# Performance work log

Measured on AMD Instinct MI355X. Metric: run time of the kernel, lower is better.

Reference implementation:

```python
import jax, jax.numpy as jnp
import numpy as np

TAU = 2.0      # LIF membrane time constant
VTH = 1.0      # spike threshold
ALPHA = 2.0    # surrogate-gradient sharpness (atan surrogate)
EPS = 1e-5     # BatchNorm eps

@jax.custom_vjp
def spike(u):
    return (u > 0.0).astype(u.dtype)

def _spike_fwd(u):
    return spike(u), u

def _spike_bwd(u, g):
    sg = ALPHA / (2.0 * (1.0 + (jnp.pi / 2.0 * ALPHA * u) ** 2))
    return (g * sg,)

spike.defvjp(_spike_fwd, _spike_bwd)

def lif_time(x):
    # x: [B,T,C,H,W] -> spikes [B,T,C,H,W]; hard-reset LIF, v0 = 0
    xT = jnp.moveaxis(x, 1, 0)  # [T,B,C,H,W]
    def step(v, xt):
        v = v + (xt - v) / TAU
        s = spike(v - VTH)
        return v * (1.0 - s), s
    _, sT = jax.lax.scan(step, jnp.zeros_like(xT[0]), xT)
    return jnp.moveaxis(sT, 0, 1)

def conv2d(x, w, stride, pad):
    return jax.lax.conv_general_dilated(
        x, w, (stride, stride), [(pad, pad), (pad, pad)],
        dimension_numbers=('NCHW', 'OIHW', 'NCHW'))

def bn(x, gamma, beta, mean, var):
    # inference-style BatchNorm2d with running stats; x: [N,C,H,W]
    inv = gamma * jax.lax.rsqrt(var + EPS)
    return x * inv[None, :, None, None] + (beta - mean * inv)[None, :, None, None]

def setup_inputs() -> dict:
    key = jax.random.key(0)
    ks = jax.random.split(key, 16)
    B, T, Cin, Cout, H, W = 16, 8, 128, 256, 56, 56
    d = {}
    d['x_spike'] = (jax.random.uniform(ks[0], (B, T, Cin, H, W)) < 0.2).astype(jnp.float32)
    d['conv1_w'] = jax.random.normal(ks[1], (Cout, Cin, 3, 3), dtype=jnp.float32) * 0.05
    d['conv2_w'] = jax.random.normal(ks[2], (Cout, Cout, 3, 3), dtype=jnp.float32) * 0.05
    d['ds_w'] = jax.random.normal(ks[3], (Cout, Cin, 1, 1), dtype=jnp.float32) * 0.05
    for i, p in enumerate(['n1', 'n2', 'nd']):
        d[p + '_gamma'] = 1.0 + 0.1 * jax.random.normal(ks[4 + i], (Cout,), dtype=jnp.float32)
        d[p + '_beta'] = 0.1 * jax.random.normal(ks[7 + i], (Cout,), dtype=jnp.float32)
        d[p + '_mean'] = 0.01 * jax.random.normal(ks[10 + i], (Cout,), dtype=jnp.float32)
        d[p + '_var'] = jax.random.uniform(ks[13 + i], (Cout,), minval=0.5, maxval=1.5)
    return d

def reference(x_spike, conv1_w, conv2_w, ds_w,
              n1_gamma, n1_beta, n1_mean, n1_var,
              n2_gamma, n2_beta, n2_mean, n2_var,
              nd_gamma, nd_beta, nd_mean, nd_var):
    B, T, Cin, H, W = x_spike.shape
    x_flat = x_spike.reshape(B * T, Cin, H, W)
    # downsample shortcut (1x1 conv stride 2 + BN)
    identity = bn(conv2d(x_flat, ds_w, 2, 0), nd_gamma, nd_beta, nd_mean, nd_var)
    # NOTE: original module runs lif_shortcut on identity but DISCARDS the result
    # (pure state side-effect); it does not affect the output, so it is omitted.
    out = bn(conv2d(x_flat, conv1_w, 2, 1), n1_gamma, n1_beta, n1_mean, n1_var)
    Cout, Ho, Wo = out.shape[1], out.shape[2], out.shape[3]
    out = lif_time(out.reshape(B, T, Cout, Ho, Wo))
    out = bn(conv2d(out.reshape(B * T, Cout, Ho, Wo), conv2_w, 1, 1),
             n2_gamma, n2_beta, n2_mean, n2_var) + identity
    return lif_time(out.reshape(B, T, Cout, Ho, Wo))
```

## Files before the change

### kernel.cpp

```cpp
#include <hip/hip_runtime.h>
#include <hip/hip_bf16.h>

#define CIN  128
#define CO   256
#define HIN  56
#define WIN  56
#define OH   28
#define OWW  28
#define P    784
#define HWIN 3136
#define PERT 200704

typedef __attribute__((ext_vector_type(8))) short bf16x8v;
typedef __attribute__((ext_vector_type(4))) float f32x4;

__device__ __forceinline__ f32x4 mfma16(bf16x8v a, bf16x8v b, f32x4 c) {
    return __builtin_amdgcn_mfma_f32_16x16x32_bf16(a, b, c, 0, 0, 0);
}

__device__ __forceinline__ void gld_lds16(const void* g, void* l) {
    __builtin_amdgcn_global_load_lds(
        (const __attribute__((address_space(1))) void*)g,
        (__attribute__((address_space(3))) void*)l, 16, 0, 0);
}

__global__ __launch_bounds__(256) void k_prep_bias(
    const float* __restrict__ g1, const float* __restrict__ b1,
    const float* __restrict__ m1, const float* __restrict__ v1,
    const float* __restrict__ g2, const float* __restrict__ b2,
    const float* __restrict__ m2, const float* __restrict__ v2,
    const float* __restrict__ gd, const float* __restrict__ bd,
    const float* __restrict__ md, const float* __restrict__ vd,
    float* __restrict__ inv1o, float* __restrict__ bias1o,
    float* __restrict__ inv2o, float* __restrict__ invdo,
    float* __restrict__ bias2o)
{
    int co = threadIdx.x;
    float inv1 = g1[co] / sqrtf(v1[co] + 1e-5f);
    float inv2 = g2[co] / sqrtf(v2[co] + 1e-5f);
    float invd = gd[co] / sqrtf(vd[co] + 1e-5f);
    inv1o[co]  = inv1;
    bias1o[co] = fmaf(-m1[co], inv1, b1[co]);
    inv2o[co]  = inv2;
    invdo[co]  = invd;
    bias2o[co] = fmaf(-m2[co], inv2, b2[co]) + fmaf(-md[co], invd, bd[co]);
}

__global__ __launch_bounds__(256) void k_prep_w2p(
    const float* __restrict__ w2, const float* __restrict__ inv2,
    unsigned short* __restrict__ hi, unsigned short* __restrict__ lo)
{
    int i = blockIdx.x * 256 + threadIdx.x;
    if (i >= 73728) return;
    int tap = i >> 13;
    int r   = i & 8191;
    int ch  = r >> 10;
    int r2  = r & 1023;
    int cf  = r2 >> 6;
    int lane = r2 & 63;
    int co  = cf * 16 + (lane & 15);
    int cib = ch * 32 + (lane >> 4) * 8;
#pragma unroll
    for (int j = 0; j < 8; j++) {
        float w = w2[((size_t)co * CO + cib + j) * 9 + tap] * inv2[co];
        __hip_bfloat16 h = __float2bfloat16(w);
        __hip_bfloat16 l = __float2bfloat16(w - __bfloat162float(h));
        hi[(size_t)i * 8 + j] = *(unsigned short*)&h;
        lo[(size_t)i * 8 + j] = *(unsigned short*)&l;
    }
}

__global__ __launch_bounds__(256) void k_prep_w1p(
    const float* __restrict__ w1, const float* __restrict__ inv1,
    unsigned short* __restrict__ hi, unsigned short* __restrict__ mid,
    unsigned short* __restrict__ lo)
{
    int i = blockIdx.x * 256 + threadIdx.x;
    if (i >= 36864) return;
    int tap = i >> 12;
    int r   = i & 4095;
    int ch  = r >> 10;
    int r2  = r & 1023;
    int cf  = r2 >> 6;
    int lane = r2 & 63;
    int co  = cf * 16 + (lane & 15);
    int cib = ch * 32 + (lane >> 4) * 8;
#pragma unroll
    for (int j = 0; j < 8; j++) {
        float w = w1[((size_t)co * CIN + cib + j) * 9 + tap] * inv1[co];
        __hip_bfloat16 h = __float2bfloat16(w);
        float r1 = w - __bfloat162float(h);
        __hip_bfloat16 m = __float2bfloat16(r1);
        float r2f = r1 - __bfloat162float(m);
        __hip_bfloat16 l = __float2bfloat16(r2f);
        hi[(size_t)i * 8 + j]  = *(unsigned short*)&h;
        mid[(size_t)i * 8 + j] = *(unsigned short*)&m;
        lo[(size_t)i * 8 + j]  = *(unsigned short*)&l;
    }
}

__global__ __launch_bounds__(256) void k_prep_wdp(
    const float* __restrict__ wd, const float* __restrict__ invd,
    unsigned short* __restrict__ hi, unsigned short* __restrict__ lo)
{
    int i = blockIdx.x * 256 + threadIdx.x;
    if (i >= 4096) return;
    int ch  = i >> 10;
    int r2  = i & 1023;
    int cf  = r2 >> 6;
    int lane = r2 & 63;
    int co  = cf * 16 + (lane & 15);
    int cib = ch * 32 + (lane >> 4) * 8;
#pragma unroll
    for (int j = 0; j < 8; j++) {
        float w = wd[(size_t)co * CIN + cib + j] * invd[co];
        __hip_bfloat16 h = __float2bfloat16(w);
        __hip_bfloat16 l = __float2bfloat16(w - __bfloat162float(h));
        hi[(size_t)i * 8 + j] = *(unsigned short*)&h;
        lo[(size_t)i * 8 + j] = *(unsigned short*)&l;
    }
}

__global__ __launch_bounds__(256) void k_pack1(
    const float* __restrict__ x, unsigned int* __restrict__ xt_p)
{
    int i = blockIdx.x * 256 + threadIdx.x;
    int pos = i % HWIN;
    int nw  = i / HWIN;
    int w   = nw & 3;
    int n   = nw >> 2;
    const float* xp = x + ((size_t)n * CIN + w * 32) * HWIN + pos;
    unsigned int word = 0;
#pragma unroll
    for (int ci = 0; ci < 32; ci++)
        if (xp[(size_t)ci * HWIN] != 0.f) word |= (1u << ci);
    xt_p[((size_t)n * HWIN + pos) * 4 + w] = word;
}

__global__ __launch_bounds__(256) void k_conv1_mfma(
    const unsigned int* __restrict__ xt_p,
    const unsigned short* __restrict__ w1hip,
    const unsigned short* __restrict__ w1midp,
    const unsigned short* __restrict__ w1lop,
    const float* __restrict__ bias1,
    float* __restrict__ out)
{
    __shared__ unsigned int XW[4 * 522];

    const int n    = blockIdx.x / 7;
    const int rt   = blockIdx.x - n * 7;
    const int r0   = rt * 4;
    const int tid  = threadIdx.x;
    const int wave = tid >> 6;
    const int lane = tid & 63;
    const int l15  = lane & 15;
    const int quad = lane >> 4;
    const int cf0  = blockIdx.y * 8 + wave * 2;

    const unsigned int* xp_n = xt_p + (size_t)n * HWIN * 4;
    for (int i = tid; i < 513; i += 256) {
        int row = i / 57, c = i - row * 57;
        int irow = 2 * r0 - 1 + row;
        int iw   = c - 1;
        uint4 val = {0u, 0u, 0u, 0u};
        if (irow >= 0 && iw >= 0)
            val = *(const uint4*)(xp_n + (size_t)(irow * WIN + iw) * 4);
        int base = row * 58 + c;
        XW[0 * 522 + base] = val.x;
        XW[1 * 522 + base] = val.y;
        XW[2 * 522 + base] = val.z;
        XW[3 * 522 + base] = val.w;
    }
    __syncthreads();

    int rr[7], cc[7];
#pragma unroll
    for (int f = 0; f < 7; f++) {
        int pos = f * 16 + l15;
        rr[f] = pos / 28;
        cc[f] = pos - rr[f] * 28;
    }

    f32x4 acc[2][7];
#pragma unroll
    for (int g = 0; g < 2; g++)
#pragma unroll
        for (int f = 0; f < 7; f++) acc[g][f] = (f32x4){0.f, 0.f, 0.f, 0.f};

    bf16x8v ch0, cm0, cl0, ch1, cm1, cl1;
    bf16x8v nh0, nm0, nl0, nh1, nm1, nl1;
    {
        size_t b0 = ((size_t)0 * 16 + cf0) * 512 + lane * 8;
        ch0 = *(const bf16x8v*)(w1hip + b0);  cm0 = *(const bf16x8v*)(w1midp + b0);
        cl0 = *(const bf16x8v*)(w1lop + b0);
        ch1 = *(const bf16x8v*)(w1hip + b0 + 512); cm1 = *(const bf16x8v*)(w1midp + b0 + 512);
        cl1 = *(const bf16x8v*)(w1lop + b0 + 512);
        nh0 = ch0; nm0 = cm0; nl0 = cl0; nh1 = ch1; nm1 = cm1; nl1 = cl1;
    }

    for (int c = 0; c < 4; c++) {
        for (int tap = 0; tap < 9; tap++) {
            int rd = c * 9 + tap;
            if (rd < 35) {
                int rn = rd + 1, cn = rn / 9, tn = rn - cn * 9;
                size_t b0 = ((size_t)(tn * 4 + cn) * 16 + cf0) * 512 + lane * 8;
                nh0 = *(const bf16x8v*)(w1hip + b0);  nm0 = *(const bf16x8v*)(w1midp + b0);
                nl0 = *(const bf16x8v*)(w1lop + b0);
                nh1 = *(const bf16x8v*)(w1hip + b0 + 512); nm1 = *(const bf16x8v*)(w1midp + b0 + 512);
                nl1 = *(const bf16x8v*)(w1lop + b0 + 512);
            }
            const int kh = tap / 3, kw = tap - kh * 3;
#pragma unroll
            for (int f = 0; f < 7; f++) {
                unsigned int word = XW[c * 522 + (2 * rr[f] + kh) * 58 + 2 * cc[f] + kw];
                unsigned int byt  = (word >> (quad * 8)) & 0xffu;
                uint4 u;
                u.x = ((byt & 1u)   ? 0x3F80u : 0u) | ((byt & 2u)   ? 0x3F800000u : 0u);
                u.y = ((byt & 4u)   ? 0x3F80u : 0u) | ((byt & 8u)   ? 0x3F800000u : 0u);
                u.z = ((byt & 16u)  ? 0x3F80u : 0u) | ((byt & 32u)  ? 0x3F800000u : 0u);
                u.w = ((byt & 64u)  ? 0x3F80u : 0u) | ((byt & 128u) ? 0x3F800000u : 0u);
                union { uint4 q; bf16x8v v; } cv;
                cv.q = u;
                acc[0][f] = mfma16(ch0, cv.v, acc[0][f]);
                acc[0][f] = mfma16(cm0, cv.v, acc[0][f]);
                acc[0][f] = mfma16(cl0, cv.v, acc[0][f]);
                acc[1][f] = mfma16(ch1, cv.v, acc[1][f]);
                acc[1][f] = mfma16(cm1, cv.v, acc[1][f]);
                acc[1][f] = mfma16(cl1, cv.v, acc[1][f]);
            }
            ch0 = nh0; cm0 = nm0; cl0 = nl0; ch1 = nh1; cm1 = nm1; cl1 = nl1;
        }
    }

#pragma unroll
    for (int g = 0; g < 2; g++)
#pragma unroll
        for (int f = 0; f < 7; f++) {
            int pg = rt * 112 + f * 16 + l15;
#pragma unroll
            for (int reg = 0; reg < 4; reg++) {
                int co = cf0 * 16 + g * 16 + quad * 4 + reg;
                out[((size_t)n * CO + co) * P + pg] = acc[g][f][reg] + bias1[co];
            }
        }
}

__global__ __launch_bounds__(256) void k_lif1t(
    const float* __restrict__ pre, unsigned short* __restrict__ st)
{
    __shared__ unsigned short T[16 * 68];
    const int b   = blockIdx.x;
    const int co0 = blockIdx.y * 64;
    const int p0  = blockIdx.z * 16;
    const int tid  = threadIdx.x;
    const int pcol = tid & 15;
    const int g    = tid >> 4;
    const int pos = p0 + g;
    const int oh  = pos / 28, ow = pos - oh * 28;
    const int f8  = ((((oh + 1) * 30 + ow + 1) >> 1) & 3);
    const int o      = (pcol & 7) >> 1;
    const int no     = o ^ f8;
    const int within = (pcol & 1) * 4;
    const int chp    = (co0 >> 5) + (pcol >> 3);
    float v[4] = {0.f, 0.f, 0.f, 0.f};
    for (int t = 0; t < 8; t++) {
        const float* src = pre + (((size_t)(b * 8 + t)) * CO + co0) * P + p0;
        unsigned short s[4];
#pragma unroll
        for (int j = 0; j < 4; j++) {
            int co = g + 16 * j;
            float xv = src[(size_t)co * P + pcol];
            v[j] = v[j] + (xv - v[j]) * 0.5f;
            bool sp = v[j] > 1.0f;
            s[j] = sp ? 0x3F80 : 0;
            if (sp) v[j] = 0.f;
        }
        __syncthreads();
#pragma unroll
        for (int j = 0; j < 4; j++) T[pcol * 68 + g + 16 * j] = s[j];
        __syncthreads();
        unsigned short* dst = st + (((size_t)(b * 8 + t) * 8 + chp) * P + pos) * 32
                               + no * 8 + within;
        ushort4 ov;
        ov.x = T[g * 68 + pcol * 4 + 0];
        ov.y = T[g * 68 + pcol * 4 + 1];
        ov.z = T[g * 68 + pcol * 4 + 2];
        ov.w = T[g * 68 + pcol * 4 + 3];
        *(ushort4*)dst = ov;
    }
}

__global__ __launch_bounds__(256) void k_conv2_mfma(
    const unsigned short* __restrict__ spike_t,
    const unsigned int* __restrict__ xt_p,
    const unsigned short* __restrict__ w2hip,
    const unsigned short* __restrict__ w2lop,
    const unsigned short* __restrict__ wdhip,
    const unsigned short* __restrict__ wdlop,
    const float* __restrict__ bias2,
    float* __restrict__ out)
{
    __shared__ unsigned short SB[2 * 5760];
    __shared__ unsigned int   XW2[4 * 112];

    const int n    = blockIdx.x / 7;
    const int rt   = blockIdx.x - n * 7;
    const int r0   = rt * 4;
    const int tid  = threadIdx.x;
    const int wave = tid >> 6;
    const int lane = tid & 63;
    const int l15  = lane & 15;
    const int quad = lane >> 4;
    const int cf0  = blockIdx.y * 8 + wave * 2;

    {
        uint4 z = {0u, 0u, 0u, 0u};
        for (int i = tid; i < 1440; i += 256) ((uint4*)SB)[i] = z;
    }
    for (int i = tid; i < 112; i += 256) {
        int r = i / 28, c = i - r * 28;
        uint4 w4 = *(const uint4*)(xt_p + ((size_t)n * HWIN
                    + (2 * (r0 + r)) * WIN + 2 * c) * 4);
        XW2[0 * 112 + i] = w4.x;
        XW2[1 * 112 + i] = w4.y;
        XW2[2 * 112 + i] = w4.z;
        XW2[3 * 112 + i] = w4.w;
    }
    __syncthreads();

    int  g_irow[3], g_lds[3];
    bool g_ok[3];
    int  g_half[3];
#pragma unroll
    for (int k = 0; k < 3; k++) {
        int idx  = wave * 3 + k;
        int row  = idx >> 1, half = idx & 1;
        int irow = r0 - 1 + row;
        g_irow[k] = irow;
        g_half[k] = half;
        g_ok[k]   = ((unsigned)irow < 28u) && (half == 0 || lane < 48);
        g_lds[k]  = row * 1920 + 64 + half * 1024;
    }
    const char* sp_n = (const char*)spike_t + (size_t)n * 8 * P * 64;

#pragma unroll
    for (int k = 0; k < 3; k++)
        if (g_ok[k])
            gld_lds16(sp_n + (size_t)g_irow[k] * 1792 + g_half[k] * 1024 + lane * 16,
                      (char*)SB + g_lds[k]);

    int rr[7], cc[7];
#pragma unroll
    for (int f = 0; f < 7; f++) {
        int pos = f * 16 + l15;
        rr[f] = pos / 28;
        cc[f] = pos - rr[f] * 28;
    }

    f32x4 acc[2][7];
#pragma unroll
    for (int g = 0; g < 2; g++)
#pragma unroll
        for (int f = 0; f < 7; f++) acc[g][f] = (f32x4){0.f, 0.f, 0.f, 0.f};

    for (int c = 0; c < 4; c++) {
        size_t b0 = ((size_t)c * 16 + cf0) * 512 + lane * 8;
        bf16x8v a0h = *(const bf16x8v*)(wdhip + b0);
        bf16x8v a0l = *(const bf16x8v*)(wdlop + b0);
        bf16x8v a1h = *(const bf16x8v*)(wdhip + b0 + 512);
        bf16x8v a1l = *(const bf16x8v*)(wdlop + b0 + 512);
#pragma unroll
        for (int f = 0; f < 7; f++) {
            unsigned int word = XW2[c * 112 + rr[f] * 28 + cc[f]];
            unsigned int byt  = (word >> (quad * 8)) & 0xffu;
            uint4 u;
            u.x = ((byt & 1u)   ? 0x3F80u : 0u) | ((byt & 2u)   ? 0x3F800000u : 0u);
            u.y = ((byt & 4u)   ? 0x3F80u : 0u) | ((byt & 8u)   ? 0x3F800000u : 0u);
            u.z = ((byt & 16u)  ? 0x3F80u : 0u) | ((byt & 32u)  ? 0x3F800000u : 0u);
            u.w = ((byt & 64u)  ? 0x3F80u : 0u) | ((byt & 128u) ? 0x3F800000u : 0u);
            union { uint4 q; bf16x8v v; } cv;
            cv.q = u;
            acc[0][f] = mfma16(a0h, cv.v, acc[0][f]);
            acc[0][f] = mfma16(a0l, cv.v, acc[0][f]);
            acc[1][f] = mfma16(a1h, cv.v, acc[1][f]);
            acc[1][f] = mfma16(a1l, cv.v, acc[1][f]);
        }
    }
    __syncthreads();

    bf16x8v ch0, cl0, ch1, cl1, nh0, nl0, nh1, nl1;
    {
        size_t b0 = ((size_t)0 * 16 + cf0) * 512 + lane * 8;
        ch0 = *(const bf16x8v*)(w2hip + b0);
        cl0 = *(const bf16x8v*)(w2lop + b0);
        ch1 = *(const bf16x8v*)(w2hip + b0 + 512);
        cl1 = *(const bf16x8v*)(w2lop + b0 + 512);
        nh0 = ch0; nl0 = cl0; nh1 = ch1; nl1 = cl1;
    }

    for (int c = 0; c < 8; c++) {
        if (c < 7) {
            const char* base = sp_n + (size_t)(c + 1) * 50176;
            char* dstb = (char*)SB + ((c + 1) & 1) * 11520;
#pragma unroll
            for (int k = 0; k < 3; k++)
                if (g_ok[k])
                    gld_lds16(base + (size_t)g_irow[k] * 1792 + g_half[k] * 1024 + lane * 16,
                              dstb + g_lds[k]);
        }
        const int bufsh = (c & 1) * 5760;
        for (int tap = 0; tap < 9; tap++) {
            int rd = c * 9 + tap;
            if (rd < 71) {
                int rn = rd + 1, cn = rn / 9, tn = rn - cn * 9;
                size_t b0 = ((size_t)(tn * 8 + cn) * 16 + cf0) * 512 + lane * 8;
                nh0 = *(const bf16x8v*)(w2hip + b0);
                nl0 = *(const bf16x8v*)(w2lop + b0);
                nh1 = *(const bf16x8v*)(w2hip + b0 + 512);
                nl1 = *(const bf16x8v*)(w2lop + b0 + 512);
            }
            const int kh = tap / 3, kw = tap - kh * 3;
#pragma unroll
            for (int f = 0; f < 7; f++) {
                int slot = (rr[f] + kh) * 30 + cc[f] + kw;
                int sw   = (slot >> 1) & 3;
                bf16x8v bfr = *(const bf16x8v*)(
                    &SB[bufsh + slot * 32 + ((quad ^ sw) * 8)]);
                acc[0][f] = mfma16(ch0, bfr, acc[0][f]);
                acc[0][f] = mfma16(cl0, bfr, acc[0][f]);
                acc[1][f] = mfma16(ch1, bfr, acc[1][f]);
                acc[1][f] = mfma16(cl1, bfr, acc[1][f]);
            }
            ch0 = nh0; cl0 = nl0; ch1 = nh1; cl1 = nl1;
        }
        __syncthreads();
    }

#pragma unroll
    for (int g = 0; g < 2; g++)
#pragma unroll
        for (int f = 0; f < 7; f++) {
            int pg = rt * 112 + f * 16 + l15;
#pragma unroll
            for (int reg = 0; reg < 4; reg++) {
                int co = cf0 * 16 + g * 16 + quad * 4 + reg;
                out[((size_t)n * CO + co) * P + pg] = acc[g][f][reg] + bias2[co];
            }
        }
}

__global__ __launch_bounds__(256) void k_lif4(const float4* __restrict__ in,
                                              float4* __restrict__ out)
{
    const int q = PERT / 4;
    const int i = blockIdx.x * 256 + threadIdx.x;
    const int b = i / q;
    const int r = i - b * q;
    const float4* pi = in  + (size_t)(b * 8) * q + r;
    float4*       po = out + (size_t)(b * 8) * q + r;
    float v0 = 0.f, v1 = 0.f, v2 = 0.f, v3 = 0.f;
#pragma unroll
    for (int t = 0; t < 8; t++) {
        float4 xt = pi[(size_t)t * q];
        float4 s;
        v0 = v0 + (xt.x - v0) * 0.5f; s.x = (v0 > 1.0f) ? 1.f : 0.f; if (v0 > 1.0f) v0 = 0.f;
        v1 = v1 + (xt.y - v1) * 0.5f; s.y = (v1 > 1.0f) ? 1.f : 0.f; if (v1 > 1.0f) v1 = 0.f;
        v2 = v2 + (xt.z - v2) * 0.5f; s.z = (v2 > 1.0f) ? 1.f : 0.f; if (v2 > 1.0f) v2 = 0.f;
        v3 = v3 + (xt.w - v3) * 0.5f; s.w = (v3 > 1.0f) ? 1.f : 0.f; if (v3 > 1.0f) v3 = 0.f;
        po[(size_t)t * q] = s;
    }
}

extern "C" void kernel_launch(void* const* d_in, const int* in_sizes, int n_in,
                              void* d_out, int out_size, void* d_ws, size_t ws_size,
                              hipStream_t stream) {
    const float* x   = (const float*)d_in[0];
    const float* w1  = (const float*)d_in[1];
    const float* w2  = (const float*)d_in[2];
    const float* wd  = (const float*)d_in[3];
    const float* n1g = (const float*)d_in[4];
    const float* n1b = (const float*)d_in[5];
    const float* n1m = (const float*)d_in[6];
    const float* n1v = (const float*)d_in[7];
    const float* n2g = (const float*)d_in[8];
    const float* n2b = (const float*)d_in[9];
    const float* n2m = (const float*)d_in[10];
    const float* n2v = (const float*)d_in[11];
    const float* ndg = (const float*)d_in[12];
    const float* ndb = (const float*)d_in[13];
    const float* ndm = (const float*)d_in[14];
    const float* ndv = (const float*)d_in[15];

    float* out = (float*)d_out;

    char* w = (char*)d_ws;
    unsigned short* spike_t = (unsigned short*)w;
    unsigned short* w2hip   = (unsigned short*)(w + 51380224);
    unsigned short* w2lop   = (unsigned short*)(w + 52559872);
    unsigned short* w1hip   = (unsigned short*)(w + 53739520);
    unsigned short* w1midp  = (unsigned short*)(w + 54329344);
    unsigned short* w1lop   = (unsigned short*)(w + 54919168);
    unsigned short* wdhip   = (unsigned short*)(w + 55508992);
    unsigned short* wdlop   = (unsigned short*)(w + 55574528);
    float*          bias2   = (float*)(w + 55640064);
    float*          bias1   = (float*)(w + 55641088);
    float*          inv1    = (float*)(w + 55642112);
    float*          inv2    = (float*)(w + 55643136);
    float*          invd    = (float*)(w + 55644160);
    unsigned int*   xt_p    = (unsigned int*)(w + 55645184);

    k_prep_bias<<<1, 256, 0, stream>>>(n1g, n1b, n1m, n1v,
                                       n2g, n2b, n2m, n2v,
                                       ndg, ndb, ndm, ndv,
                                       inv1, bias1, inv2, invd, bias2);
    k_prep_w2p<<<288, 256, 0, stream>>>(w2, inv2, w2hip, w2lop);
    k_prep_w1p<<<144, 256, 0, stream>>>(w1, inv1, w1hip, w1midp, w1lop);
    k_prep_wdp<<<16, 256, 0, stream>>>(wd, invd, wdhip, wdlop);

    k_pack1<<<(128 * 4 * HWIN) / 256, 256, 0, stream>>>(x, xt_p);
    k_conv1_mfma<<<dim3(896, 2), 256, 0, stream>>>(
        xt_p, w1hip, w1midp, w1lop, bias1, out);
    k_lif1t<<<dim3(16, 4, 49), 256, 0, stream>>>(out, spike_t);
    k_conv2_mfma<<<dim3(896, 2), 256, 0, stream>>>(
        spike_t, xt_p, w2hip, w2lop, wdhip, wdlop, bias2, out);
    k_lif4<<<(16 * (PERT / 4)) / 256, 256, 0, stream>>>(
        (const float4*)out, (float4*)out);
}
```

Baseline: 820.0 us.

## Compute all 256 output channels per conv2 block to halve spike-tile reloads

The conv2 kernel now has each wave cover four 16-channel groups instead of two, so one block produces all 256 output channels and the grid's y-dimension of 2 is removed. Each block loads the spike input tiles and packed shortcut input into LDS once for all channels, where two blocks previously loaded the same data. In exchange, accumulator and weight-register use per thread roughly doubles, which can lower occupancy or cause spills. The grid also shrinks to 896 blocks.

```diff
diff --git a/kernel.cpp b/kernel.cpp
--- a/kernel.cpp
+++ b/kernel.cpp
@@ -311,7 +311,7 @@
     const int lane = tid & 63;
     const int l15  = lane & 15;
     const int quad = lane >> 4;
-    const int cf0  = blockIdx.y * 8 + wave * 2;
+    const int cf0  = wave * 4;
 
     {
         uint4 z = {0u, 0u, 0u, 0u};
@@ -357,18 +357,20 @@
         cc[f] = pos - rr[f] * 28;
     }
 
-    f32x4 acc[2][7];
-#pragma unroll
-    for (int g = 0; g < 2; g++)
+    f32x4 acc[4][7];
+#pragma unroll
+    for (int g = 0; g < 4; g++)
 #pragma unroll
         for (int f = 0; f < 7; f++) acc[g][f] = (f32x4){0.f, 0.f, 0.f, 0.f};
 
     for (int c = 0; c < 4; c++) {
         size_t b0 = ((size_t)c * 16 + cf0) * 512 + lane * 8;
-        bf16x8v a0h = *(const bf16x8v*)(wdhip + b0);
-        bf16x8v a0l = *(const bf16x8v*)(wdlop + b0);
-        bf16x8v a1h = *(const bf16x8v*)(wdhip + b0 + 512);
-        bf16x8v a1l = *(const bf16x8v*)(wdlop + b0 + 512);
+        bf16x8v ah[4], al[4];
+#pragma unroll
+        for (int g = 0; g < 4; g++) {
+            ah[g] = *(const bf16x8v*)(wdhip + b0 + g * 512);
+            al[g] = *(const bf16x8v*)(wdlop + b0 + g * 512);
+        }
 #pragma unroll
         for (int f = 0; f < 7; f++) {
             unsigned int word = XW2[c * 112 + rr[f] * 28 + cc[f]];
@@ -380,22 +382,25 @@
             u.w = ((byt & 64u)  ? 0x3F80u : 0u) | ((byt & 128u) ? 0x3F800000u : 0u);
             union { uint4 q; bf16x8v v; } cv;
             cv.q = u;
-            acc[0][f] = mfma16(a0h, cv.v, acc[0][f]);
-            acc[0][f] = mfma16(a0l, cv.v, acc[0][f]);
-            acc[1][f] = mfma16(a1h, cv.v, acc[1][f]);
-            acc[1][f] = mfma16(a1l, cv.v, acc[1][f]);
+#pragma unroll
+            for (int g = 0; g < 4; g++) {
+                acc[g][f] = mfma16(ah[g], cv.v, acc[g][f]);
+                acc[g][f] = mfma16(al[g], cv.v, acc[g][f]);
+            }
         }
     }
     __syncthreads();
 
-    bf16x8v ch0, cl0, ch1, cl1, nh0, nl0, nh1, nl1;
+    bf16x8v cw[8], nx[8];
     {
         size_t b0 = ((size_t)0 * 16 + cf0) * 512 + lane * 8;
-        ch0 = *(const bf16x8v*)(w2hip + b0);
-        cl0 = *(const bf16x8v*)(w2lop + b0);
-        ch1 = *(const bf16x8v*)(w2hip + b0 + 512);
-        cl1 = *(const bf16x8v*)(w2lop + b0 + 512);
-        nh0 = ch0; nl0 = cl0; nh1 = ch1; nl1 = cl1;
+#pragma unroll
+        for (int g = 0; g < 4; g++) {
+            cw[2 * g]     = *(const bf16x8v*)(w2hip + b0 + g * 512);
+            cw[2 * g + 1] = *(const bf16x8v*)(w2lop + b0 + g * 512);
+            nx[2 * g]     = cw[2 * g];
+            nx[2 * g + 1] = cw[2 * g + 1];
+        }
     }
 
     for (int c = 0; c < 8; c++) {
@@ -414,10 +419,11 @@
             if (rd < 71) {
                 int rn = rd + 1, cn = rn / 9, tn = rn - cn * 9;
                 size_t b0 = ((size_t)(tn * 8 + cn) * 16 + cf0) * 512 + lane * 8;
-                nh0 = *(const bf16x8v*)(w2hip + b0);
-                nl0 = *(const bf16x8v*)(w2lop + b0);
-                nh1 = *(const bf16x8v*)(w2hip + b0 + 512);
-                nl1 = *(const bf16x8v*)(w2lop + b0 + 512);
+#pragma unroll
+                for (int g = 0; g < 4; g++) {
+                    nx[2 * g]     = *(const bf16x8v*)(w2hip + b0 + g * 512);
+                    nx[2 * g + 1] = *(const bf16x8v*)(w2lop + b0 + g * 512);
+                }
             }
             const int kh = tap / 3, kw = tap - kh * 3;
 #pragma unroll
@@ -426,24 +432,26 @@
                 int sw   = (slot >> 1) & 3;
                 bf16x8v bfr = *(const bf16x8v*)(
                     &SB[bufsh + slot * 32 + ((quad ^ sw) * 8)]);
-                acc[0][f] = mfma16(ch0, bfr, acc[0][f]);
-                acc[0][f] = mfma16(cl0, bfr, acc[0][f]);
-                acc[1][f] = mfma16(ch1, bfr, acc[1][f]);
-                acc[1][f] = mfma16(cl1, bfr, acc[1][f]);
-            }
-            ch0 = nh0; cl0 = nl0; ch1 = nh1; cl1 = nl1;
+#pragma unroll
+                for (int g = 0; g < 4; g++) {
+                    acc[g][f] = mfma16(cw[2 * g], bfr, acc[g][f]);
+                    acc[g][f] = mfma16(cw[2 * g + 1], bfr, acc[g][f]);
+                }
+            }
+#pragma unroll
+            for (int j = 0; j < 8; j++) cw[j] = nx[j];
         }
         __syncthreads();
     }
 
 #pragma unroll
-    for (int g = 0; g < 2; g++)
+    for (int g = 0; g < 4; g++)
 #pragma unroll
         for (int f = 0; f < 7; f++) {
             int pg = rt * 112 + f * 16 + l15;
 #pragma unroll
             for (int reg = 0; reg < 4; reg++) {
-                int co = cf0 * 16 + g * 16 + quad * 4 + reg;
+                int co = (cf0 + g) * 16 + quad * 4 + reg;
                 out[((size_t)n * CO + co) * P + pg] = acc[g][f][reg] + bias2[co];
             }
         }
@@ -521,7 +529,7 @@
     k_conv1_mfma<<<dim3(896, 2), 256, 0, stream>>>(
         xt_p, w1hip, w1midp, w1lop, bias1, out);
     k_lif1t<<<dim3(16, 4, 49), 256, 0, stream>>>(out, spike_t);
-    k_conv2_mfma<<<dim3(896, 2), 256, 0, stream>>>(
+    k_conv2_mfma<<<dim3(896), 256, 0, stream>>>(
         spike_t, xt_p, w2hip, w2lop, wdhip, wdlop, bias2, out);
     k_lif4<<<(16 * (PERT / 4)) / 256, 256, 0, stream>>>(
         (const float4*)out, (float4*)out);
```

Measured after the change: 713.7 us (median of 3 runs). 1.15x faster.
